# Kernel tuning notes

Measured on AMD Instinct MI355X. Metric: run time of the kernel, lower is better.

The kernel has to match this reference:

```python
import jax, jax.numpy as jnp
import numpy as np

B, S, D = 4, 4096, 1024
H, EXPAND, DCONV = 8, 2, 4
DI = D * EXPAND           # d_inner = 2048
HD = DI // H              # head_dim = 256
LN_EPS = 1e-5


def setup_inputs() -> dict:
    key = jax.random.key(0)
    ks = jax.random.split(key, 6)
    scale = lambda fan_in: 1.0 / np.sqrt(fan_in)
    return {
        "x": jax.random.normal(ks[0], (B, S, D), dtype=jnp.float32),
        "norm_w": jnp.ones((D,), dtype=jnp.float32),
        "norm_b": jnp.zeros((D,), dtype=jnp.float32),
        "in_proj_w": jax.random.normal(ks[1], (2 * DI, D), dtype=jnp.float32) * scale(D),
        "conv_w": jax.random.normal(ks[2], (DI, 1, DCONV), dtype=jnp.float32) * scale(DCONV),
        "conv_b": jax.random.normal(ks[3], (DI,), dtype=jnp.float32) * 0.02,
        "out_proj_w": jax.random.normal(ks[4], (D, DI), dtype=jnp.float32) * scale(DI),
        "log_alpha": jax.random.uniform(ks[5], (H,), dtype=jnp.float32,
                                        minval=np.log(0.1), maxval=np.log(0.99)),
    }


def reference(x, norm_w, norm_b, in_proj_w, conv_w, conv_b, out_proj_w, log_alpha):
    residual = x
    # LayerNorm
    mu = jnp.mean(x, axis=-1, keepdims=True)
    var = jnp.var(x, axis=-1, keepdims=True)
    xn = (x - mu) * jax.lax.rsqrt(var + LN_EPS) * norm_w + norm_b
    # input projection -> [B, S, 2*DI]
    xz = jnp.einsum("bsd,ed->bse", xn, in_proj_w)
    x_path, gate = xz[..., :DI], xz[..., DI:]
    # causal depthwise conv1d (torch pads d_conv-1 both sides then slices [:S])
    kernel = jnp.transpose(conv_w, (2, 1, 0))  # [DCONV, 1, DI] (WIO)
    x_path = jax.lax.conv_general_dilated(
        x_path, kernel, window_strides=(1,), padding=[(DCONV - 1, 0)],
        dimension_numbers=("NWC", "WIO", "NWC"), feature_group_count=DI,
    ) + conv_b
    # multi-head scalar-decay linear recurrence: y_t = alpha*y_{t-1} + x_t
    xh = x_path.reshape(B, S, H, HD)
    alpha = jax.nn.sigmoid(log_alpha)[:, None]  # [H, 1]

    def step(y, xt):
        y = alpha * y + xt
        return y, y

    y0 = jnp.zeros((B, H, HD), dtype=x.dtype)
    _, ys = jax.lax.scan(step, y0, jnp.transpose(xh, (1, 0, 2, 3)))  # [S, B, H, HD]
    x_path = jnp.transpose(ys, (1, 0, 2, 3)).reshape(B, S, DI)
    # gate + output projection (dropout in eval mode = identity)
    x_path = jax.nn.silu(x_path) * gate
    out = jnp.einsum("bse,de->bsd", x_path, out_proj_w)
    return out + residual
```

## Files before the change

### kernel.cpp

```cpp
#include <hip/hip_runtime.h>
#include <hip/hip_bf16.h>
#include <cstdint>

#define Bb 4
#define Ss 4096
#define Dd 1024
#define Hh 8
#define DI 2048
#define HD 256
#define XZN 4096
#define Mtot 16384
#define NCH 128
#define CHUNK 32

typedef __bf16 bf16_t;
typedef __bf16 bf16x8 __attribute__((ext_vector_type(8)));
typedef __bf16 bf16x4 __attribute__((ext_vector_type(4)));
typedef float f32x4 __attribute__((ext_vector_type(4)));

__device__ __forceinline__ float sigmoidf_(float x) { return 1.f / (1.f + __expf(-x)); }

__device__ __forceinline__ void async_ld16(void* lds, const void* g) {
  __builtin_amdgcn_global_load_lds(
      (const __attribute__((address_space(1))) void*)(uintptr_t)g,
      (__attribute__((address_space(3))) void*)(uint32_t)(uintptr_t)lds,
      16, 0, 0);
}

__global__ __launch_bounds__(256) void cvt_kernel(const float* __restrict__ s,
                                                  bf16_t* __restrict__ d) {
  const int i = blockIdx.x * 256 + threadIdx.x;
  const float4 v = ((const float4*)s)[i];
  bf16_t* o = d + 4 * (size_t)i;
  o[0] = (bf16_t)v.x; o[1] = (bf16_t)v.y; o[2] = (bf16_t)v.z; o[3] = (bf16_t)v.w;
}

__global__ __launch_bounds__(256) void ln_kernel(const float* __restrict__ x,
                                                 const float* __restrict__ w,
                                                 const float* __restrict__ b,
                                                 bf16_t* __restrict__ xn) {
  __shared__ float red[8];
  const int row = blockIdx.x;
  const float4 v = ((const float4*)(x + (size_t)row * Dd))[threadIdx.x];
  float s  = v.x + v.y + v.z + v.w;
  float s2 = v.x * v.x + v.y * v.y + v.z * v.z + v.w * v.w;
  #pragma unroll
  for (int off = 32; off; off >>= 1) { s += __shfl_down(s, off); s2 += __shfl_down(s2, off); }
  const int wave = threadIdx.x >> 6, lane = threadIdx.x & 63;
  if (lane == 0) { red[wave * 2] = s; red[wave * 2 + 1] = s2; }
  __syncthreads();
  if (threadIdx.x == 0) {
    float S = 0.f, S2 = 0.f;
    for (int i = 0; i < 4; ++i) { S += red[i * 2]; S2 += red[i * 2 + 1]; }
    red[0] = S; red[1] = S2;
  }
  __syncthreads();
  const float mean = red[0] * (1.f / Dd);
  const float var  = red[1] * (1.f / Dd) - mean * mean;
  const float rstd = rsqrtf(var + 1e-5f);
  const float4 wv = ((const float4*)w)[threadIdx.x];
  const float4 bv = ((const float4*)b)[threadIdx.x];
  bf16_t* o = xn + (size_t)row * Dd + threadIdx.x * 4;
  o[0] = (bf16_t)((v.x - mean) * rstd * wv.x + bv.x);
  o[1] = (bf16_t)((v.y - mean) * rstd * wv.y + bv.y);
  o[2] = (bf16_t)((v.z - mean) * rstd * wv.z + bv.z);
  o[3] = (bf16_t)((v.w - mean) * rstd * wv.w + bv.w);
}

template <int ADD_RES>
__global__ __launch_bounds__(512, 2) void gemm256(const bf16_t* __restrict__ A,
                                                  const bf16_t* __restrict__ Bw,
                                                  void* __restrict__ Cv,
                                                  const float* __restrict__ res,
                                                  int M, int N, int K) {
  __shared__ __align__(16) char LDS[131072];
  const int tid = threadIdx.x;
  const int wave = tid >> 6, lane = tid & 63;
  const int wm = wave >> 2, wn = wave & 3;

  const int nbx = gridDim.x;
  const int nwg = nbx * gridDim.y;
  const int bid0 = blockIdx.y * nbx + blockIdx.x;
  const int cpx = nwg >> 3;
  const int bid = (bid0 & 7) * cpx + (bid0 >> 3);
  const int bm = bid / nbx, bn = bid % nbx;

  f32x4 acc[8][4];
  #pragma unroll
  for (int i = 0; i < 8; ++i)
    #pragma unroll
    for (int j = 0; j < 4; ++j) acc[i][j] = (f32x4){0.f, 0.f, 0.f, 0.f};

  const int scg = (lane & 3) ^ ((lane >> 3) & 3);
  const bf16_t* Ag = A  + (size_t)(bm * 256 + wave * 16 + (lane >> 2)) * K + scg * 8;
  const bf16_t* Bg = Bw + (size_t)(bn * 256 + wave * 16 + (lane >> 2)) * K + scg * 8;
  const size_t rowK128 = (size_t)128 * K;
  char* const LDSw = LDS + wave * 1024;

  const int fr = lane & 15, fq = lane >> 4;
  int aoff[8], boff[4];
  #pragma unroll
  for (int mt = 0; mt < 8; ++mt) {
    const int row = wm * 128 + mt * 16 + fr;
    aoff[mt] = row * 64 + ((fq ^ ((row >> 1) & 3)) << 4);
  }
  #pragma unroll
  for (int nt = 0; nt < 4; ++nt) {
    const int row = wn * 64 + nt * 16 + fr;
    boff[nt] = row * 64 + ((fq ^ ((row >> 1) & 3)) << 4);
  }

  const int NT = K >> 6;

#define STG(u, mat, ks) do {                                              \
    char* d_ = LDSw + ((u) & 1) * 65536 + (mat) * 32768 + (ks) * 16384;   \
    const bf16_t* s_ = (mat) ? Bg : Ag;                                   \
    const int ko_ = (u) * 64 + (ks) * 32;                                 \
    async_ld16(d_,        s_ + ko_);                                      \
    async_ld16(d_ + 8192, s_ + rowK128 + ko_);                            \
  } while (0)

#define RDA(DST, bufb, ks, g) do {                                        \
    _Pragma("unroll")                                                     \
    for (int i_ = 0; i_ < 4; ++i_)                                        \
      DST[i_] = *(const bf16x8*)(LDS + (bufb) * 65536 + (ks) * 16384 + aoff[(g) * 4 + i_]); \
  } while (0)

#define RDB(DST, bufb, ks) do {                                           \
    _Pragma("unroll")                                                     \
    for (int i_ = 0; i_ < 4; ++i_)                                        \
      DST[i_] = *(const bf16x8*)(LDS + (bufb) * 65536 + 32768 + (ks) * 16384 + boff[i_]); \
  } while (0)

#define MM(AF, BF, g) do {                                                \
    __builtin_amdgcn_s_setprio(1);                                        \
    _Pragma("unroll")                                                     \
    for (int m_ = 0; m_ < 4; ++m_)                                        \
      _Pragma("unroll")                                                   \
      for (int n_ = 0; n_ < 4; ++n_)                                      \
        acc[(g) * 4 + m_][n_] = __builtin_amdgcn_mfma_f32_16x16x32_bf16(  \
            AF[m_], BF[n_], acc[(g) * 4 + m_][n_], 0, 0, 0);              \
    __builtin_amdgcn_s_setprio(0);                                        \
  } while (0)

#define LGKM0 do { asm volatile("s_waitcnt lgkmcnt(0)" ::: "memory");     \
    __builtin_amdgcn_sched_barrier(0); } while (0)
#define VMB4 do { asm volatile("s_waitcnt vmcnt(4)" ::: "memory");        \
    __builtin_amdgcn_s_barrier(); } while (0)
#define VMB0 do { asm volatile("s_waitcnt vmcnt(0)" ::: "memory");        \
    __builtin_amdgcn_s_barrier(); } while (0)

  STG(0, 0, 0); STG(0, 1, 0); STG(0, 0, 1); STG(0, 1, 1);
  bf16x8 af[4], ag[4], bfk[4];

  for (int t = 0; t < NT - 1; ++t) {
    const int cb = t & 1;
    VMB4;
    RDB(bfk, cb, 0); RDA(af, cb, 0, 0);
    STG(t + 1, 0, 0);
    LGKM0; MM(af, bfk, 0);
    RDA(ag, cb, 0, 1);
    STG(t + 1, 1, 0);
    LGKM0; MM(ag, bfk, 1);
    VMB4;
    RDB(bfk, cb, 1); RDA(af, cb, 1, 0);
    STG(t + 1, 0, 1);
    LGKM0; MM(af, bfk, 0);
    RDA(ag, cb, 1, 1);
    STG(t + 1, 1, 1);
    LGKM0; MM(ag, bfk, 1);
  }
  {
    const int cb = (NT - 1) & 1;
    VMB4;
    RDB(bfk, cb, 0); RDA(af, cb, 0, 0);
    LGKM0; MM(af, bfk, 0);
    RDA(ag, cb, 0, 1);
    LGKM0; MM(ag, bfk, 1);
    VMB0;
    RDB(bfk, cb, 1); RDA(af, cb, 1, 0);
    LGKM0; MM(af, bfk, 0);
    RDA(ag, cb, 1, 1);
    LGKM0; MM(ag, bfk, 1);
  }

#undef STG
#undef RDA
#undef RDB
#undef MM
#undef LGKM0
#undef VMB4
#undef VMB0

  const int m0 = bm * 256 + wm * 128 + fq * 4;
  const int n0 = bn * 256 + wn * 64 + fr;
  #pragma unroll
  for (int mt = 0; mt < 8; ++mt)
    #pragma unroll
    for (int nt = 0; nt < 4; ++nt)
      #pragma unroll
      for (int r = 0; r < 4; ++r) {
        const size_t m = (size_t)(m0 + mt * 16 + r);
        const size_t n = (size_t)(n0 + nt * 16);
        if (ADD_RES)
          ((float*)Cv)[m * N + n] = acc[mt][nt][r] + res[m * N + n];
        else
          ((bf16_t*)Cv)[m * N + n] = (bf16_t)acc[mt][nt][r];
      }
}

__global__ __launch_bounds__(256) void scanA_kernel(const bf16_t* __restrict__ xz,
                                                    const float* __restrict__ conv_w,
                                                    const float* __restrict__ conv_b,
                                                    const float* __restrict__ log_alpha,
                                                    float* __restrict__ carry) {
  const int half  = blockIdx.x & 1;
  const int chunk = (blockIdx.x >> 1) & (NCH - 1);
  const int b     = blockIdx.x >> 8;
  const int ch    = half * 1024 + threadIdx.x * 4;
  const float alpha = sigmoidf_(log_alpha[ch >> 8]);
  float w[4][4], bias[4];
  #pragma unroll
  for (int j = 0; j < 4; ++j) {
    const float4 cw = ((const float4*)conv_w)[ch + j];
    w[j][0] = cw.x; w[j][1] = cw.y; w[j][2] = cw.z; w[j][3] = cw.w;
    bias[j] = conv_b[ch + j];
  }
  const int s0 = chunk * CHUNK;
  const size_t base = ((size_t)b * Ss + s0) * XZN + ch;
  float x3[4] = {0,0,0,0}, x2[4] = {0,0,0,0}, x1[4] = {0,0,0,0}, y[4] = {0,0,0,0};
  if (chunk > 0) {
    const bf16x4 v3 = *(const bf16x4*)(xz + base - 3 * (size_t)XZN);
    const bf16x4 v2 = *(const bf16x4*)(xz + base - 2 * (size_t)XZN);
    const bf16x4 v1 = *(const bf16x4*)(xz + base - 1 * (size_t)XZN);
    #pragma unroll
    for (int j = 0; j < 4; ++j) { x3[j] = (float)v3[j]; x2[j] = (float)v2[j]; x1[j] = (float)v1[j]; }
  }
  #pragma unroll 4
  for (int t = 0; t < CHUNK; ++t) {
    const bf16x4 v = *(const bf16x4*)(xz + base + (size_t)t * XZN);
    #pragma unroll
    for (int j = 0; j < 4; ++j) {
      const float xc = (float)v[j];
      const float cv = bias[j] + w[j][0] * x3[j] + w[j][1] * x2[j] + w[j][2] * x1[j] + w[j][3] * xc;
      x3[j] = x2[j]; x2[j] = x1[j]; x1[j] = xc;
      y[j] = fmaf(alpha, y[j], cv);
    }
  }
  *(float4*)(carry + ((size_t)b * NCH + chunk) * DI + ch) =
      make_float4(y[0], y[1], y[2], y[3]);
}

__global__ __launch_bounds__(256) void scanB_kernel(const float* __restrict__ carry,
                                                    float* __restrict__ carryin,
                                                    const float* __restrict__ log_alpha) {
  __shared__ float S[8][32];
  const int b   = blockIdx.x >> 6;
  const int chg = blockIdx.x & 63;
  const int cg  = threadIdx.x >> 5;
  const int chl = threadIdx.x & 31;
  const int ch  = chg * 32 + chl;
  const float alpha = sigmoidf_(log_alpha[ch >> 8]);
  const float lal  = log2f(alpha);
  const float aL   = exp2f((float)CHUNK * lal);
  const float aL16 = exp2f((float)(CHUNK * 16) * lal);
  const size_t base = ((size_t)b * NCH + cg * 16) * DI + ch;
  float v[16];
  #pragma unroll
  for (int i = 0; i < 16; ++i) v[i] = carry[base + (size_t)i * DI];
  float Sl = v[0];
  #pragma unroll
  for (int i = 1; i < 16; ++i) Sl = fmaf(aL, Sl, v[i]);
  S[cg][chl] = Sl;
  __syncthreads();
  float P = 0.f;
  for (int h = 0; h < cg; ++h) P = fmaf(aL16, P, S[h][chl]);
  #pragma unroll
  for (int i = 0; i < 16; ++i) {
    carryin[base + (size_t)i * DI] = P;
    P = fmaf(aL, P, v[i]);
  }
}

__global__ __launch_bounds__(256) void scanC_kernel(const bf16_t* __restrict__ xz,
                                                    const float* __restrict__ conv_w,
                                                    const float* __restrict__ conv_b,
                                                    const float* __restrict__ log_alpha,
                                                    const float* __restrict__ carryin,
                                                    bf16_t* __restrict__ act) {
  const int half  = blockIdx.x & 1;
  const int chunk = (blockIdx.x >> 1) & (NCH - 1);
  const int b     = blockIdx.x >> 8;
  const int ch    = half * 1024 + threadIdx.x * 4;
  const float alpha = sigmoidf_(log_alpha[ch >> 8]);
  float w[4][4], bias[4];
  #pragma unroll
  for (int j = 0; j < 4; ++j) {
    const float4 cw = ((const float4*)conv_w)[ch + j];
    w[j][0] = cw.x; w[j][1] = cw.y; w[j][2] = cw.z; w[j][3] = cw.w;
    bias[j] = conv_b[ch + j];
  }
  const int s0 = chunk * CHUNK;
  const size_t base = ((size_t)b * Ss + s0) * XZN + ch;
  float x3[4] = {0,0,0,0}, x2[4] = {0,0,0,0}, x1[4] = {0,0,0,0}, y[4];
  const float4 cin = *(const float4*)(carryin + ((size_t)b * NCH + chunk) * DI + ch);
  y[0] = cin.x; y[1] = cin.y; y[2] = cin.z; y[3] = cin.w;
  if (chunk > 0) {
    const bf16x4 v3 = *(const bf16x4*)(xz + base - 3 * (size_t)XZN);
    const bf16x4 v2 = *(const bf16x4*)(xz + base - 2 * (size_t)XZN);
    const bf16x4 v1 = *(const bf16x4*)(xz + base - 1 * (size_t)XZN);
    #pragma unroll
    for (int j = 0; j < 4; ++j) { x3[j] = (float)v3[j]; x2[j] = (float)v2[j]; x1[j] = (float)v1[j]; }
  }
  const size_t abase = ((size_t)b * Ss + s0) * DI + ch;
  #pragma unroll 4
  for (int t = 0; t < CHUNK; ++t) {
    const bf16x4 v = *(const bf16x4*)(xz + base + (size_t)t * XZN);
    const bf16x4 gv = *(const bf16x4*)(xz + base + (size_t)t * XZN + DI);
    bf16x4 ov;
    #pragma unroll
    for (int j = 0; j < 4; ++j) {
      const float xc = (float)v[j];
      const float cv = bias[j] + w[j][0] * x3[j] + w[j][1] * x2[j] + w[j][2] * x1[j] + w[j][3] * xc;
      x3[j] = x2[j]; x2[j] = x1[j]; x1[j] = xc;
      y[j] = fmaf(alpha, y[j], cv);
      const float o = y[j] * (1.f / (1.f + __expf(-y[j]))) * (float)gv[j];
      ov[j] = (bf16_t)o;
    }
    *(bf16x4*)(act + abase + (size_t)t * DI) = ov;
  }
}

extern "C" void kernel_launch(void* const* d_in, const int* in_sizes, int n_in,
                              void* d_out, int out_size, void* d_ws, size_t ws_size,
                              hipStream_t stream) {
  const float* x          = (const float*)d_in[0];
  const float* norm_w     = (const float*)d_in[1];
  const float* norm_b     = (const float*)d_in[2];
  const float* in_proj_w  = (const float*)d_in[3];
  const float* conv_w     = (const float*)d_in[4];
  const float* conv_b     = (const float*)d_in[5];
  const float* out_proj_w = (const float*)d_in[6];
  const float* log_alpha  = (const float*)d_in[7];
  float* out = (float*)d_out;

  char* ws = (char*)d_ws;
  bf16_t* xn     = (bf16_t*)(ws);
  bf16_t* w_in   = (bf16_t*)(ws + 33554432);
  bf16_t* w_out  = (bf16_t*)(ws + 41943040);
  bf16_t* xz     = (bf16_t*)(ws + 46137344);
  bf16_t* act    = (bf16_t*)(ws + 180355072);
  float*  carry   = (float*)(ws);
  float*  carryin = (float*)(ws + 4194304);

  cvt_kernel<<<4096, 256, 0, stream>>>(in_proj_w, w_in);
  cvt_kernel<<<2048, 256, 0, stream>>>(out_proj_w, w_out);
  ln_kernel<<<Mtot, 256, 0, stream>>>(x, norm_w, norm_b, xn);

  dim3 g1(XZN / 256, Mtot / 256);
  gemm256<0><<<g1, 512, 0, stream>>>(xn, w_in, xz, nullptr, Mtot, XZN, Dd);

  scanA_kernel<<<Bb * NCH * 2, 256, 0, stream>>>(xz, conv_w, conv_b, log_alpha, carry);
  scanB_kernel<<<Bb * 64, 256, 0, stream>>>(carry, carryin, log_alpha);
  scanC_kernel<<<Bb * NCH * 2, 256, 0, stream>>>(xz, conv_w, conv_b, log_alpha, carryin, act);

  dim3 g2(Dd / 256, Mtot / 256);
  gemm256<1><<<g2, 512, 0, stream>>>(act, w_out, out, x, Mtot, Dd, DI);
}
```

Before: 392.2 us.

## Restructure GEMM main loop into deeper async-prefetch pipeline with phase barriers

Rewrites the bf16 GEMM K-loop to process two K-tiles per iteration, issuing global->LDS async loads further ahead (prefetching into the next buffer slot at half-tile granularity) with vmcnt(6) waits instead of vmcnt(4). Each MFMA phase is bracketed by workgroup barriers so LDS reads and compute are synchronised per phase. Prologue issues loads before accumulator/offset setup to hide latency. Adds more barriers per iteration, which risks extra sync overhead, and relies on buffer-reuse ordering being correct.

```diff
diff --git a/kernel.cpp b/kernel.cpp
--- a/kernel.cpp
+++ b/kernel.cpp
@@ -85,32 +85,11 @@
   const int bid = (bid0 & 7) * cpx + (bid0 >> 3);
   const int bm = bid / nbx, bn = bid % nbx;
 
-  f32x4 acc[8][4];
-  #pragma unroll
-  for (int i = 0; i < 8; ++i)
-    #pragma unroll
-    for (int j = 0; j < 4; ++j) acc[i][j] = (f32x4){0.f, 0.f, 0.f, 0.f};
-
   const int scg = (lane & 3) ^ ((lane >> 3) & 3);
   const bf16_t* Ag = A  + (size_t)(bm * 256 + wave * 16 + (lane >> 2)) * K + scg * 8;
   const bf16_t* Bg = Bw + (size_t)(bn * 256 + wave * 16 + (lane >> 2)) * K + scg * 8;
   const size_t rowK128 = (size_t)128 * K;
   char* const LDSw = LDS + wave * 1024;
-
-  const int fr = lane & 15, fq = lane >> 4;
-  int aoff[8], boff[4];
-  #pragma unroll
-  for (int mt = 0; mt < 8; ++mt) {
-    const int row = wm * 128 + mt * 16 + fr;
-    aoff[mt] = row * 64 + ((fq ^ ((row >> 1) & 3)) << 4);
-  }
-  #pragma unroll
-  for (int nt = 0; nt < 4; ++nt) {
-    const int row = wn * 64 + nt * 16 + fr;
-    boff[nt] = row * 64 + ((fq ^ ((row >> 1) & 3)) << 4);
-  }
-
-  const int NT = K >> 6;
 
 #define STG(u, mat, ks) do {                                              \
     char* d_ = LDSw + ((u) & 1) * 65536 + (mat) * 32768 + (ks) * 16384;   \
@@ -120,6 +99,31 @@
     async_ld16(d_ + 8192, s_ + rowK128 + ko_);                            \
   } while (0)
 
+  const int NT = K >> 6;
+  const int NI = NT >> 1;
+
+  STG(0, 1, 0); STG(0, 0, 0); STG(0, 1, 1); STG(0, 0, 1);
+  STG(1, 1, 0); STG(1, 0, 0); STG(1, 1, 1);
+
+  f32x4 acc[8][4];
+  #pragma unroll
+  for (int i = 0; i < 8; ++i)
+    #pragma unroll
+    for (int j = 0; j < 4; ++j) acc[i][j] = (f32x4){0.f, 0.f, 0.f, 0.f};
+
+  const int fr = lane & 15, fq = lane >> 4;
+  int aoff[8], boff[4];
+  #pragma unroll
+  for (int mt = 0; mt < 8; ++mt) {
+    const int row = wm * 128 + mt * 16 + fr;
+    aoff[mt] = row * 64 + ((fq ^ ((row >> 1) & 3)) << 4);
+  }
+  #pragma unroll
+  for (int nt = 0; nt < 4; ++nt) {
+    const int row = wn * 64 + nt * 16 + fr;
+    boff[nt] = row * 64 + ((fq ^ ((row >> 1) & 3)) << 4);
+  }
+
 #define RDA(DST, bufb, ks, g) do {                                        \
     _Pragma("unroll")                                                     \
     for (int i_ = 0; i_ < 4; ++i_)                                        \
@@ -132,65 +136,57 @@
       DST[i_] = *(const bf16x8*)(LDS + (bufb) * 65536 + 32768 + (ks) * 16384 + boff[i_]); \
   } while (0)
 
+#define RDAB(BQ, AQ, par, ks) do { RDB(BQ, par, ks); RDA(AQ, par, ks, 0); } while (0)
+
 #define MM(AF, BF, g) do {                                                \
-    __builtin_amdgcn_s_setprio(1);                                        \
     _Pragma("unroll")                                                     \
     for (int m_ = 0; m_ < 4; ++m_)                                        \
       _Pragma("unroll")                                                   \
       for (int n_ = 0; n_ < 4; ++n_)                                      \
         acc[(g) * 4 + m_][n_] = __builtin_amdgcn_mfma_f32_16x16x32_bf16(  \
             AF[m_], BF[n_], acc[(g) * 4 + m_][n_], 0, 0, 0);              \
-    __builtin_amdgcn_s_setprio(0);                                        \
-  } while (0)
-
-#define LGKM0 do { asm volatile("s_waitcnt lgkmcnt(0)" ::: "memory");     \
-    __builtin_amdgcn_sched_barrier(0); } while (0)
-#define VMB4 do { asm volatile("s_waitcnt vmcnt(4)" ::: "memory");        \
-    __builtin_amdgcn_s_barrier(); } while (0)
-#define VMB0 do { asm volatile("s_waitcnt vmcnt(0)" ::: "memory");        \
-    __builtin_amdgcn_s_barrier(); } while (0)
-
-  STG(0, 0, 0); STG(0, 1, 0); STG(0, 0, 1); STG(0, 1, 1);
-  bf16x8 af[4], ag[4], bfk[4];
-
-  for (int t = 0; t < NT - 1; ++t) {
-    const int cb = t & 1;
-    VMB4;
-    RDB(bfk, cb, 0); RDA(af, cb, 0, 0);
-    STG(t + 1, 0, 0);
-    LGKM0; MM(af, bfk, 0);
-    RDA(ag, cb, 0, 1);
-    STG(t + 1, 1, 0);
-    LGKM0; MM(ag, bfk, 1);
-    VMB4;
-    RDB(bfk, cb, 1); RDA(af, cb, 1, 0);
-    STG(t + 1, 0, 1);
-    LGKM0; MM(af, bfk, 0);
-    RDA(ag, cb, 1, 1);
-    STG(t + 1, 1, 1);
-    LGKM0; MM(ag, bfk, 1);
-  }
-  {
-    const int cb = (NT - 1) & 1;
-    VMB4;
-    RDB(bfk, cb, 0); RDA(af, cb, 0, 0);
-    LGKM0; MM(af, bfk, 0);
-    RDA(ag, cb, 0, 1);
-    LGKM0; MM(ag, bfk, 1);
-    VMB0;
-    RDB(bfk, cb, 1); RDA(af, cb, 1, 0);
-    LGKM0; MM(af, bfk, 0);
-    RDA(ag, cb, 1, 1);
-    LGKM0; MM(ag, bfk, 1);
-  }
+  } while (0)
+
+#define VM6 asm volatile("s_waitcnt vmcnt(6)" ::: "memory")
+#define VM0 asm volatile("s_waitcnt vmcnt(0)" ::: "memory")
+
+#define PHX(MMS) do {                                                     \
+    __builtin_amdgcn_s_barrier();                                         \
+    asm volatile("s_waitcnt lgkmcnt(0)" ::: "memory");                    \
+    __builtin_amdgcn_sched_barrier(0);                                    \
+    __builtin_amdgcn_s_setprio(1); MMS; __builtin_amdgcn_s_setprio(0);    \
+    __builtin_amdgcn_s_barrier();                                         \
+  } while (0)
+
+#define ITER(tt, FULL, VM4STMT) do {                                      \
+    const int t_ = (tt);                                                  \
+    RDAB(bq, aq, 0, 0); STG(t_ + 1, 0, 1);            PHX(MM(aq,  bq, 0)); \
+    RDA(aq2, 0, 0, 1);  if (FULL) STG(t_ + 2, 1, 0);  PHX(MM(aq2, bq, 1)); \
+    RDAB(bq, aq, 0, 1); if (FULL) STG(t_ + 2, 0, 0);  PHX(MM(aq,  bq, 0)); \
+    RDA(aq2, 0, 1, 1);  if (FULL) STG(t_ + 2, 1, 1);  VM4STMT; PHX(MM(aq2, bq, 1)); \
+    RDAB(bq, aq, 1, 0); if (FULL) STG(t_ + 2, 0, 1);  PHX(MM(aq,  bq, 0)); \
+    RDA(aq2, 1, 0, 1);  if (FULL) STG(t_ + 3, 1, 0);  PHX(MM(aq2, bq, 1)); \
+    RDAB(bq, aq, 1, 1); if (FULL) STG(t_ + 3, 0, 0);  PHX(MM(aq,  bq, 0)); \
+    RDA(aq2, 1, 1, 1);  if (FULL) { STG(t_ + 3, 1, 1); VM6; }  PHX(MM(aq2, bq, 1)); \
+  } while (0)
+
+  bf16x8 aq[4], aq2[4], bq[4];
+
+  VM6;
+  __builtin_amdgcn_s_barrier();
+
+  for (int i = 0; i < NI - 1; ++i) ITER(2 * i, 1, VM6);
+  ITER(NT - 2, 0, VM0);
 
 #undef STG
 #undef RDA
 #undef RDB
+#undef RDAB
 #undef MM
-#undef LGKM0
-#undef VMB4
-#undef VMB0
+#undef VM6
+#undef VM0
+#undef PHX
+#undef ITER
 
   const int m0 = bm * 256 + wm * 128 + fq * 4;
   const int n0 = bn * 256 + wn * 64 + fr;
```

Result: no change. 397.6 us (+1.4%).

## Switch GEMM to 32x32x16 MFMA tiles and merge weight conversion kernels

Applied to the files above, without the earlier changes.

The GEMM inner loop now issues 32x32x16 bf16 MFMA instructions on 4x2 tiles of 16-wide accumulators instead of 16x16x32 on 8x4 tiles. LDS fragment reads and the epilogue index mapping are rewritten to match. The aim is fewer MFMA issues and fewer LDS reads per FLOP, since the larger instruction reuses each loaded fragment over more outputs. Separately, the two weight fp32-to-bf16 conversion launches are merged into one kernel to cut launch overhead. The new LDS swizzle addressing and epilogue layout carry a correctness risk if the XOR offsets do not match the 32x32 operand layout.

```diff
diff --git a/kernel.cpp b/kernel.cpp
--- a/kernel.cpp
+++ b/kernel.cpp
@@ -17,6 +17,7 @@
 typedef __bf16 bf16x8 __attribute__((ext_vector_type(8)));
 typedef __bf16 bf16x4 __attribute__((ext_vector_type(4)));
 typedef float f32x4 __attribute__((ext_vector_type(4)));
+typedef float f32x16 __attribute__((ext_vector_type(16)));
 
 __device__ __forceinline__ float sigmoidf_(float x) { return 1.f / (1.f + __expf(-x)); }
 
@@ -27,11 +28,17 @@
       16, 0, 0);
 }
 
-__global__ __launch_bounds__(256) void cvt_kernel(const float* __restrict__ s,
-                                                  bf16_t* __restrict__ d) {
-  const int i = blockIdx.x * 256 + threadIdx.x;
+__global__ __launch_bounds__(256) void cvt2_kernel(const float* __restrict__ a,
+                                                   bf16_t* __restrict__ da,
+                                                   const float* __restrict__ b,
+                                                   bf16_t* __restrict__ db) {
+  const int na = (2 * DI * Dd) / 4;
+  int i = blockIdx.x * 256 + threadIdx.x;
+  const float* s;
+  bf16_t* o;
+  if (i < na) { s = a; o = da + 4 * (size_t)i; }
+  else        { i -= na; s = b; o = db + 4 * (size_t)i; }
   const float4 v = ((const float4*)s)[i];
-  bf16_t* o = d + 4 * (size_t)i;
   o[0] = (bf16_t)v.x; o[1] = (bf16_t)v.y; o[2] = (bf16_t)v.z; o[3] = (bf16_t)v.w;
 }
 
@@ -85,32 +92,11 @@
   const int bid = (bid0 & 7) * cpx + (bid0 >> 3);
   const int bm = bid / nbx, bn = bid % nbx;
 
-  f32x4 acc[8][4];
-  #pragma unroll
-  for (int i = 0; i < 8; ++i)
-    #pragma unroll
-    for (int j = 0; j < 4; ++j) acc[i][j] = (f32x4){0.f, 0.f, 0.f, 0.f};
-
   const int scg = (lane & 3) ^ ((lane >> 3) & 3);
   const bf16_t* Ag = A  + (size_t)(bm * 256 + wave * 16 + (lane >> 2)) * K + scg * 8;
   const bf16_t* Bg = Bw + (size_t)(bn * 256 + wave * 16 + (lane >> 2)) * K + scg * 8;
   const size_t rowK128 = (size_t)128 * K;
   char* const LDSw = LDS + wave * 1024;
-
-  const int fr = lane & 15, fq = lane >> 4;
-  int aoff[8], boff[4];
-  #pragma unroll
-  for (int mt = 0; mt < 8; ++mt) {
-    const int row = wm * 128 + mt * 16 + fr;
-    aoff[mt] = row * 64 + ((fq ^ ((row >> 1) & 3)) << 4);
-  }
-  #pragma unroll
-  for (int nt = 0; nt < 4; ++nt) {
-    const int row = wn * 64 + nt * 16 + fr;
-    boff[nt] = row * 64 + ((fq ^ ((row >> 1) & 3)) << 4);
-  }
-
-  const int NT = K >> 6;
 
 #define STG(u, mat, ks) do {                                              \
     char* d_ = LDSw + ((u) & 1) * 65536 + (mat) * 32768 + (ks) * 16384;   \
@@ -120,27 +106,50 @@
     async_ld16(d_ + 8192, s_ + rowK128 + ko_);                            \
   } while (0)
 
-#define RDA(DST, bufb, ks, g) do {                                        \
-    _Pragma("unroll")                                                     \
-    for (int i_ = 0; i_ < 4; ++i_)                                        \
-      DST[i_] = *(const bf16x8*)(LDS + (bufb) * 65536 + (ks) * 16384 + aoff[(g) * 4 + i_]); \
-  } while (0)
-
-#define RDB(DST, bufb, ks) do {                                           \
-    _Pragma("unroll")                                                     \
-    for (int i_ = 0; i_ < 4; ++i_)                                        \
-      DST[i_] = *(const bf16x8*)(LDS + (bufb) * 65536 + 32768 + (ks) * 16384 + boff[i_]); \
-  } while (0)
-
-#define MM(AF, BF, g) do {                                                \
-    __builtin_amdgcn_s_setprio(1);                                        \
-    _Pragma("unroll")                                                     \
-    for (int m_ = 0; m_ < 4; ++m_)                                        \
-      _Pragma("unroll")                                                   \
-      for (int n_ = 0; n_ < 4; ++n_)                                      \
-        acc[(g) * 4 + m_][n_] = __builtin_amdgcn_mfma_f32_16x16x32_bf16(  \
-            AF[m_], BF[n_], acc[(g) * 4 + m_][n_], 0, 0, 0);              \
-    __builtin_amdgcn_s_setprio(0);                                        \
+  const int NT = K >> 6;
+
+  STG(0, 0, 0); STG(0, 1, 0); STG(0, 0, 1); STG(0, 1, 1);
+
+  f32x16 acc[4][2];
+  #pragma unroll
+  for (int i = 0; i < 4; ++i)
+    #pragma unroll
+    for (int j = 0; j < 2; ++j)
+      #pragma unroll
+      for (int e = 0; e < 16; ++e) acc[i][j][e] = 0.f;
+
+  const int lr = lane & 31, hi = lane >> 5;
+  int aoff[4], boff[2];
+  #pragma unroll
+  for (int mt = 0; mt < 4; ++mt) {
+    const int row = wm * 128 + mt * 32 + lr;
+    aoff[mt] = row * 64 + ((hi ^ ((row >> 1) & 3)) << 4);
+  }
+  #pragma unroll
+  for (int nt = 0; nt < 2; ++nt) {
+    const int row = wn * 64 + nt * 32 + lr;
+    boff[nt] = row * 64 + ((hi ^ ((row >> 1) & 3)) << 4);
+  }
+
+#define RDB2(B0, B1, bufb, ks, k2) do {                                             \
+    B0 = *(const bf16x8*)(LDS + (bufb) * 65536 + 32768 + (ks) * 16384 + (boff[0] ^ ((k2) * 32))); \
+    B1 = *(const bf16x8*)(LDS + (bufb) * 65536 + 32768 + (ks) * 16384 + (boff[1] ^ ((k2) * 32))); \
+  } while (0)
+
+#define RDA4(AF, bufb, ks, k2) do {                                                 \
+    _Pragma("unroll")                                                               \
+    for (int i_ = 0; i_ < 4; ++i_)                                                  \
+      AF[i_] = *(const bf16x8*)(LDS + (bufb) * 65536 + (ks) * 16384 + (aoff[i_] ^ ((k2) * 32))); \
+  } while (0)
+
+#define MM8(AF, B0, B1) do {                                                        \
+    __builtin_amdgcn_s_setprio(1);                                                  \
+    _Pragma("unroll")                                                               \
+    for (int m_ = 0; m_ < 4; ++m_) {                                                \
+      acc[m_][0] = __builtin_amdgcn_mfma_f32_32x32x16_bf16(AF[m_], B0, acc[m_][0], 0, 0, 0); \
+      acc[m_][1] = __builtin_amdgcn_mfma_f32_32x32x16_bf16(AF[m_], B1, acc[m_][1], 0, 0, 0); \
+    }                                                                               \
+    __builtin_amdgcn_s_setprio(0);                                                  \
   } while (0)
 
 #define LGKM0 do { asm volatile("s_waitcnt lgkmcnt(0)" ::: "memory");     \
@@ -150,58 +159,48 @@
 #define VMB0 do { asm volatile("s_waitcnt vmcnt(0)" ::: "memory");        \
     __builtin_amdgcn_s_barrier(); } while (0)
 
-  STG(0, 0, 0); STG(0, 1, 0); STG(0, 0, 1); STG(0, 1, 1);
-  bf16x8 af[4], ag[4], bfk[4];
-
-  for (int t = 0; t < NT - 1; ++t) {
-    const int cb = t & 1;
-    VMB4;
-    RDB(bfk, cb, 0); RDA(af, cb, 0, 0);
-    STG(t + 1, 0, 0);
-    LGKM0; MM(af, bfk, 0);
-    RDA(ag, cb, 0, 1);
-    STG(t + 1, 1, 0);
-    LGKM0; MM(ag, bfk, 1);
-    VMB4;
-    RDB(bfk, cb, 1); RDA(af, cb, 1, 0);
-    STG(t + 1, 0, 1);
-    LGKM0; MM(af, bfk, 0);
-    RDA(ag, cb, 1, 1);
-    STG(t + 1, 1, 1);
-    LGKM0; MM(ag, bfk, 1);
-  }
-  {
-    const int cb = (NT - 1) & 1;
-    VMB4;
-    RDB(bfk, cb, 0); RDA(af, cb, 0, 0);
-    LGKM0; MM(af, bfk, 0);
-    RDA(ag, cb, 0, 1);
-    LGKM0; MM(ag, bfk, 1);
-    VMB0;
-    RDB(bfk, cb, 1); RDA(af, cb, 1, 0);
-    LGKM0; MM(af, bfk, 0);
-    RDA(ag, cb, 1, 1);
-    LGKM0; MM(ag, bfk, 1);
-  }
+#define ITER(tt, FULL, VMID) do {                                         \
+    const int t_ = (tt); const int cb_ = t_ & 1;                          \
+    VMB4;                                        \
+    RDB2(b0, b1, cb_, 0, 0); RDB2(c0, c1, cb_, 0, 1); RDA4(af, cb_, 0, 0); \
+    if (FULL) STG(t_ + 1, 0, 0);                                          \
+    LGKM0; MM8(af, b0, b1);                                               \
+    RDA4(ag, cb_, 0, 1);                                                  \
+    if (FULL) STG(t_ + 1, 1, 0);                                          \
+    LGKM0; MM8(ag, c0, c1);                                               \
+    VMID;                                        \
+    RDB2(b0, b1, cb_, 1, 0); RDB2(c0, c1, cb_, 1, 1); RDA4(af, cb_, 1, 0); \
+    if (FULL) STG(t_ + 1, 0, 1);                                          \
+    LGKM0; MM8(af, b0, b1);                                               \
+    RDA4(ag, cb_, 1, 1);                                                  \
+    if (FULL) STG(t_ + 1, 1, 1);                                          \
+    LGKM0; MM8(ag, c0, c1);                                               \
+  } while (0)
+
+  bf16x8 af[4], ag[4], b0, b1, c0, c1;
+
+  for (int t = 0; t < NT - 1; ++t) ITER(t, 1, VMB4);
+  ITER(NT - 1, 0, VMB0);
 
 #undef STG
-#undef RDA
-#undef RDB
-#undef MM
+#undef RDB2
+#undef RDA4
+#undef MM8
 #undef LGKM0
 #undef VMB4
 #undef VMB0
-
-  const int m0 = bm * 256 + wm * 128 + fq * 4;
-  const int n0 = bn * 256 + wn * 64 + fr;
-  #pragma unroll
-  for (int mt = 0; mt < 8; ++mt)
-    #pragma unroll
-    for (int nt = 0; nt < 4; ++nt)
+#undef ITER
+
+  const int m0 = bm * 256 + wm * 128 + hi * 4;
+  const int n0 = bn * 256 + wn * 64 + lr;
+  #pragma unroll
+  for (int mt = 0; mt < 4; ++mt)
+    #pragma unroll
+    for (int nt = 0; nt < 2; ++nt)
       #pragma unroll
-      for (int r = 0; r < 4; ++r) {
-        const size_t m = (size_t)(m0 + mt * 16 + r);
-        const size_t n = (size_t)(n0 + nt * 16);
+      for (int r = 0; r < 16; ++r) {
+        const size_t m = (size_t)(m0 + mt * 32 + (r & 3) + 8 * (r >> 2));
+        const size_t n = (size_t)(n0 + nt * 32);
         if (ADD_RES)
           ((float*)Cv)[m * N + n] = acc[mt][nt][r] + res[m * N + n];
         else
@@ -353,8 +352,7 @@
   float*  carry   = (float*)(ws);
   float*  carryin = (float*)(ws + 4194304);
 
-  cvt_kernel<<<4096, 256, 0, stream>>>(in_proj_w, w_in);
-  cvt_kernel<<<2048, 256, 0, stream>>>(out_proj_w, w_out);
+  cvt2_kernel<<<6144, 256, 0, stream>>>(in_proj_w, w_in, out_proj_w, w_out);
   ln_kernel<<<Mtot, 256, 0, stream>>>(x, norm_w, norm_b, xn);
 
   dim3 g1(XZN / 256, Mtot / 256);
```

Result: slower. 418.3 us (+6.6%).
